# Kernel optimization log

Measured on AMD Instinct MI355X. Metric: run time of the kernel, lower is better.

Reference implementation:

```python
import jax, jax.numpy as jnp
import numpy as np

NEG_SLOPE = 0.2  # PyG GATConv default leaky_relu slope
EPS = 1e-16     # PyG softmax denominator epsilon


def gat_conv(x, src, dst, W, att_src, att_dst, bias, concat, num_nodes):
    """PyG-style GATConv (eval mode, dropout disabled).
    x: [N, F_in]; W: [F_in, H*C]; att_src/att_dst: [H, C]; bias: [H*C] or [C].
    Messages flow src -> dst; softmax is per destination node."""
    H, C = att_src.shape
    h = (x @ W).reshape(num_nodes, H, C)                      # [N,H,C]
    a_src = jnp.sum(h * att_src[None], axis=-1)               # [N,H]
    a_dst = jnp.sum(h * att_dst[None], axis=-1)               # [N,H]
    e = jax.nn.leaky_relu(a_src[src] + a_dst[dst], NEG_SLOPE) # [E,H]
    # numerically-stable segment softmax over edges grouped by dst
    m = jax.ops.segment_max(e, dst, num_segments=num_nodes)   # [N,H]
    ex = jnp.exp(e - m[dst])                                  # [E,H]
    s = jax.ops.segment_sum(ex, dst, num_segments=num_nodes)  # [N,H]
    alpha = ex / (s[dst] + EPS)                               # [E,H]
    msg = h[src] * alpha[..., None]                           # [E,H,C]
    out = jax.ops.segment_sum(msg, dst, num_segments=num_nodes)  # [N,H,C]
    if concat:
        out = out.reshape(num_nodes, H * C)
    else:
        out = out.mean(axis=1)                                # [N,C]
    return out + bias, alpha


def setup_inputs() -> dict:
    key = jax.random.key(0)
    ks = jax.random.split(key, 20)
    N, E = 50000, 500000
    F_node = 128       # num_node_features
    SED = 128          # sentence_embedding_dim
    HID = 64           # hidden_channels
    H = 2              # num_heads

    def g(k, shape, scale=0.05):
        return jax.random.normal(k, shape, dtype=jnp.float32) * scale

    return {
        "x": jax.random.normal(ks[0], (N, SED), dtype=jnp.float32),
        "edge_index": jax.random.randint(ks[1], (2, E), 0, N, dtype=jnp.int64),
        "cls_emb": jax.random.normal(ks[2], (768,), dtype=jnp.float32),
        # fc0: Linear(768, SED)
        "fc0_w": g(ks[3], (SED, 768)), "fc0_b": g(ks[4], (SED,)),
        # conv1: GATConv(2*SED -> HID, heads=H, concat=True)
        "W1": g(ks[5], (2 * SED, H * HID)),
        "att_src1": g(ks[6], (H, HID)), "att_dst1": g(ks[7], (H, HID)),
        "bias1": g(ks[8], (H * HID,)),
        # conv2: GATConv(H*HID -> F_node, heads=H, concat=False)
        "W2": g(ks[9], (H * HID, H * F_node)),
        "att_src2": g(ks[10], (H, F_node)), "att_dst2": g(ks[11], (H, F_node)),
        "bias2": g(ks[12], (F_node,)),
        # edge MLP head
        "fc2_w": g(ks[13], (F_node, 2 * F_node)), "fc2_b": g(ks[14], (F_node,)),
        "fc3_w": g(ks[15], (1, F_node)), "fc3_b": g(ks[16], (1,)),
    }


def reference(x, edge_index, cls_emb, fc0_w, fc0_b,
              W1, att_src1, att_dst1, bias1,
              W2, att_src2, att_dst2, bias2,
              fc2_w, fc2_b, fc3_w, fc3_b):
    N = x.shape[0]
    src, dst = edge_index[0], edge_index[1]
    # sentence embedding projection + broadcast-concat to every node
    sent = fc0_w @ cls_emb + fc0_b                                # [SED]
    h = jnp.concatenate([x, jnp.broadcast_to(sent, (N, sent.shape[0]))], axis=1)
    h, _ = gat_conv(h, src, dst, W1, att_src1, att_dst1, bias1, True, N)
    h = jax.nn.elu(h)
    h, _ = gat_conv(h, src, dst, W2, att_src2, att_dst2, bias2, False, N)
    # edge head: gather endpoints, concat, MLP, sigmoid
    edge_input = jnp.concatenate([h[src], h[dst]], axis=1)        # [E, 2*F]
    z = jax.nn.relu(edge_input @ fc2_w.T + fc2_b)                 # [E, F]
    logits = z @ fc3_w.T + fc3_b                                  # [E, 1]
    return jax.nn.sigmoid(logits)
```

## Files before the change

kernel.cpp:

```cpp
#include <hip/hip_runtime.h>
#include <hip/hip_bf16.h>
#include <math.h>


typedef short short8 __attribute__((ext_vector_type(8)));
typedef float floatx4 __attribute__((ext_vector_type(4)));
typedef float v2f __attribute__((ext_vector_type(2)));
typedef unsigned uint2v __attribute__((ext_vector_type(2)));

__device__ __forceinline__ float wave_allreduce_sum(float v) {
    #pragma unroll
    for (int off = 1; off < 64; off <<= 1) v += __shfl_xor(v, off, 64);
    return v;
}
__device__ __forceinline__ float bf16lo(unsigned u) {
    unsigned x = u << 16; return __builtin_bit_cast(float, x);
}
__device__ __forceinline__ float bf16hi(unsigned u) {
    unsigned x = u & 0xFFFF0000u; return __builtin_bit_cast(float, x);
}
__device__ __forceinline__ v2f bfpair(unsigned v) {
    uint2v t; t.x = v << 16; t.y = v & 0xFFFF0000u;
    return __builtin_bit_cast(v2f, t);
}
__device__ __forceinline__ unsigned short bfbits(float f) {
    return __builtin_bit_cast(unsigned short, __float2bfloat16(f));
}
__device__ __forceinline__ unsigned packbf(float a, float b) {
    return ((unsigned)bfbits(b) << 16) | (unsigned)bfbits(a);
}
__device__ __forceinline__ float lrelu(float v) { return v > 0.f ? v : 0.2f * v; }

__global__ void prep_kernel(const float* __restrict__ cls, const float* __restrict__ fc0_w,
                            const float* __restrict__ fc0_b, const float* __restrict__ W1,
                            const float* __restrict__ W2, const float* __restrict__ fc2_w,
                            float* __restrict__ c1,
                            __hip_bfloat16* __restrict__ w1frag,
                            __hip_bfloat16* __restrict__ w2frag,
                            __hip_bfloat16* __restrict__ fc2frag) {
    int tid = threadIdx.x;
    if (blockIdx.x == 0) {
        __shared__ float s_sent[128];
        if (tid < 128) {
            float acc = fc0_b[tid];
            const float* row = fc0_w + (size_t)tid * 768;
            for (int k = 0; k < 768; ++k) acc += row[k] * cls[k];
            s_sent[tid] = acc;
        }
        __syncthreads();
        if (tid < 128) {
            float acc = 0.f;
            for (int k = 0; k < 128; ++k) acc += s_sent[k] * W1[(128 + k) * 128 + tid];
            c1[tid] = acc;
        }
    }
    int gstride = gridDim.x * blockDim.x;
    int g = blockIdx.x * blockDim.x + tid;
    for (int i = g; i < 16384; i += gstride) {
        int j = i & 7, l = (i >> 3) & 63, nt = (i >> 9) & 7, kt = (i >> 12) & 3;
        int k = kt * 32 + (l >> 4) * 8 + j;
        int n = nt * 16 + (l & 15);
        w1frag[i] = __float2bfloat16(W1[k * 128 + n]);
    }
    for (int i = g; i < 32768; i += gstride) {
        int j = i & 7, l = (i >> 3) & 63, nt = (i >> 9) & 15, kt = (i >> 13) & 3;
        int k = kt * 32 + (l >> 4) * 8 + j;
        int n = nt * 16 + (l & 15);
        w2frag[i] = __float2bfloat16(W2[k * 256 + n]);
    }
    for (int i = g; i < 32768; i += gstride) {
        int j = i & 7, l = (i >> 3) & 63, nt = (i >> 9) & 15, kt = (i >> 13) & 3;
        int k = kt * 32 + (l >> 4) * 8 + j;
        int n = nt * 16 + (l & 15);
        float v = (n < 128) ? fc2_w[n * 256 + k] : fc2_w[(n - 128) * 256 + 128 + k];
        fc2frag[i] = __float2bfloat16(v);
    }
}

__global__ void count_kernel(const int* __restrict__ dst, int* __restrict__ counts, int E) {
    int e = blockIdx.x * blockDim.x + threadIdx.x;
    if (e < E) atomicAdd(&counts[dst[e]], 1);
}

__global__ void __launch_bounds__(1024) scan_kernel(const int* __restrict__ counts,
                                                    int* __restrict__ row, int* __restrict__ woff,
                                                    int N, int E) {
    int tid = threadIdx.x, lane = tid & 63, wv = tid >> 6;
    __shared__ int wsum[16];
    __shared__ int carry;
    if (tid == 0) carry = 0;
    __syncthreads();
    for (int base = 0; base < N; base += 1024) {
        int v = (base + tid < N) ? counts[base + tid] : 0;
        int x = v;
        #pragma unroll
        for (int off = 1; off < 64; off <<= 1) {
            int t = __shfl_up(x, off, 64);
            if (lane >= off) x += t;
        }
        if (lane == 63) wsum[wv] = x;
        __syncthreads();
        if (wv == 0 && lane < 16) {
            int y = wsum[lane];
            #pragma unroll
            for (int off = 1; off < 16; off <<= 1) {
                int t = __shfl_up(y, off, 64);
                if (lane >= off) y += t;
            }
            wsum[lane] = y;
        }
        __syncthreads();
        int wexcl = (wv == 0) ? 0 : wsum[wv - 1];
        int excl = carry + wexcl + x - v;
        if (base + tid < N) { row[base + tid] = excl; woff[base + tid] = excl; }
        __syncthreads();
        if (tid == 0) carry += wsum[15];
        __syncthreads();
    }
    if (tid == 0) row[N] = E;
}

__global__ void scatter_kernel(const int* __restrict__ src, const int* __restrict__ dst,
                               int* __restrict__ woff, int* __restrict__ srcs, int E) {
    int e = blockIdx.x * blockDim.x + threadIdx.x;
    if (e < E) {
        int pos = atomicAdd(&woff[dst[e]], 1);
        srcs[pos] = src[e];
    }
}

__global__ void __launch_bounds__(256) gemm1_mfma_kernel(
        const float* __restrict__ x, const __hip_bfloat16* __restrict__ wfrag,
        const float* __restrict__ c1, const float* __restrict__ att_s, const float* __restrict__ att_d,
        __hip_bfloat16* __restrict__ h1bf, float* __restrict__ a_src, float* __restrict__ a_dst, int N) {
    int lane = threadIdx.x & 63, wv = threadIdx.x >> 6;
    int lo = lane & 15, quad = lane >> 4;
    int rowbase = (blockIdx.x * 4 + wv) * 16;
    if (rowbase >= N) return;
    int arow = rowbase + lo; if (arow >= N) arow = N - 1;
    const float* ap = x + (size_t)arow * 128 + quad * 8;
    floatx4 acc[8];
    #pragma unroll
    for (int nt = 0; nt < 8; ++nt) acc[nt] = (floatx4){0.f, 0.f, 0.f, 0.f};
    const short8* bf = (const short8*)wfrag;
    #pragma unroll
    for (int kt = 0; kt < 4; ++kt) {
        float4 fa = *(const float4*)(ap + kt * 32);
        float4 fb = *(const float4*)(ap + kt * 32 + 4);
        short8 a;
        a[0] = (short)bfbits(fa.x); a[1] = (short)bfbits(fa.y);
        a[2] = (short)bfbits(fa.z); a[3] = (short)bfbits(fa.w);
        a[4] = (short)bfbits(fb.x); a[5] = (short)bfbits(fb.y);
        a[6] = (short)bfbits(fb.z); a[7] = (short)bfbits(fb.w);
        #pragma unroll
        for (int nt = 0; nt < 8; ++nt)
            acc[nt] = __builtin_amdgcn_mfma_f32_16x16x32_bf16(a, bf[(kt * 8 + nt) * 64 + lane], acc[nt], 0, 0, 0);
    }
    float ps0[4] = {0,0,0,0}, ps1[4] = {0,0,0,0}, pd0[4] = {0,0,0,0}, pd1[4] = {0,0,0,0};
    #pragma unroll
    for (int nt = 0; nt < 8; ++nt) {
        int ch = nt * 16 + lo;
        float cv = c1[ch], as_v = att_s[ch], ad_v = att_d[ch];
        #pragma unroll
        for (int r = 0; r < 4; ++r) {
            int row = rowbase + quad * 4 + r;
            float val = acc[nt][r] + cv;
            if (row < N) ((unsigned short*)h1bf)[(size_t)row * 128 + ch] = bfbits(val);
            if (nt < 4) { ps0[r] += val * as_v; pd0[r] += val * ad_v; }
            else        { ps1[r] += val * as_v; pd1[r] += val * ad_v; }
        }
    }
    #pragma unroll
    for (int r = 0; r < 4; ++r) {
        int row = rowbase + quad * 4 + r;
        float v0 = ps0[r], v1 = ps1[r], v2 = pd0[r], v3 = pd1[r];
        #pragma unroll
        for (int off = 1; off < 16; off <<= 1) {
            v0 += __shfl_xor(v0, off, 64); v1 += __shfl_xor(v1, off, 64);
            v2 += __shfl_xor(v2, off, 64); v3 += __shfl_xor(v3, off, 64);
        }
        if (lo == 0 && row < N) {
            a_src[row * 2 + 0] = v0; a_src[row * 2 + 1] = v1;
            a_dst[row * 2 + 0] = v2; a_dst[row * 2 + 1] = v3;
        }
    }
}

__global__ void __launch_bounds__(256) agg1_csr_kernel(
        const int* __restrict__ row, const int* __restrict__ srcs,
        const float* __restrict__ a_src, const float* __restrict__ a_dst,
        const unsigned* __restrict__ h1u, const float* __restrict__ bias1,
        unsigned* __restrict__ hmid_u, int N) {
    int d = blockIdx.x * 4 + (threadIdx.x >> 6);
    if (d >= N) return;
    int lane = threadIdx.x & 63;
    int beg = row[d], end = row[d + 1];
    int g = lane >> 4, q = lane & 15;
    float2 adp = ((const float2*)a_dst)[d];
    float den0 = 0.f, den1 = 0.f;
    v2f facc2[4];
    #pragma unroll
    for (int m = 0; m < 4; ++m) facc2[m] = (v2f){0.f, 0.f};
    for (int b = beg; b < end; b += 64) {
        int i = b + lane;
        int s = 0; float e0 = 0.f, e1 = 0.f;
        if (i < end) {
            s = srcs[i];
            float2 as = ((const float2*)a_src)[s];
            e0 = __expf(lrelu(as.x + adp.x));
            e1 = __expf(lrelu(as.y + adp.y));
            den0 += e0; den1 += e1;
        }
        int cnt = min(64, end - b);
        int rounds = (cnt + 3) >> 2;
        float w0 = __shfl(e0, g, 64);
        float w1 = __shfl(e1, g, 64);
        int   sj = __shfl(s,  g, 64);
        float wgt = (q < 8) ? w0 : w1;
        uint4 u = ((const uint4*)(h1u + (size_t)sj * 64))[q];
        for (int j = 0; j < rounds; ++j) {
            int sl2 = 4 * j + 4 + g; sl2 = sl2 > 63 ? 63 : sl2;
            float w0n = __shfl(e0, sl2, 64);
            float w1n = __shfl(e1, sl2, 64);
            int   sjn = __shfl(s,  sl2, 64);
            uint4 un = ((const uint4*)(h1u + (size_t)sjn * 64))[q];
            float wgtn = (q < 8) ? w0n : w1n;
            facc2[0] += bfpair(u.x) * wgt;
            facc2[1] += bfpair(u.y) * wgt;
            facc2[2] += bfpair(u.z) * wgt;
            facc2[3] += bfpair(u.w) * wgt;
            u = un; wgt = wgtn;
        }
    }
    den0 = wave_allreduce_sum(den0);
    den1 = wave_allreduce_sum(den1);
    #pragma unroll
    for (int m = 0; m < 4; ++m) {
        facc2[m].x += __shfl_xor(facc2[m].x, 16, 64);
        facc2[m].y += __shfl_xor(facc2[m].y, 16, 64);
        facc2[m].x += __shfl_xor(facc2[m].x, 32, 64);
        facc2[m].y += __shfl_xor(facc2[m].y, 32, 64);
    }
    if (lane < 16) {
        float inv = (lane < 8) ? 1.f / (den0 + 1e-16f) : 1.f / (den1 + 1e-16f);
        int c0 = 8 * lane;
        float v[8];
        #pragma unroll
        for (int m = 0; m < 4; ++m) {
            float va = facc2[m].x * inv + bias1[c0 + 2 * m];
            float vb = facc2[m].y * inv + bias1[c0 + 2 * m + 1];
            v[2 * m]     = va > 0.f ? va : expm1f(va);
            v[2 * m + 1] = vb > 0.f ? vb : expm1f(vb);
        }
        uint4 o;
        o.x = packbf(v[0], v[1]); o.y = packbf(v[2], v[3]);
        o.z = packbf(v[4], v[5]); o.w = packbf(v[6], v[7]);
        ((uint4*)(hmid_u + (size_t)d * 64))[lane] = o;
    }
}

__global__ void __launch_bounds__(256) gemm2_mfma_kernel(
        const __hip_bfloat16* __restrict__ hmid, const __hip_bfloat16* __restrict__ wfrag,
        const float* __restrict__ att_s, const float* __restrict__ att_d,
        __hip_bfloat16* __restrict__ h2pre, float* __restrict__ a_src, float* __restrict__ a_dst, int N) {
    int lane = threadIdx.x & 63, wv = threadIdx.x >> 6;
    int lo = lane & 15, quad = lane >> 4;
    int rowbase = (blockIdx.x * 4 + wv) * 16;
    if (rowbase >= N) return;
    int arow = rowbase + lo; if (arow >= N) arow = N - 1;
    const __hip_bfloat16* ap = hmid + (size_t)arow * 128 + quad * 8;
    floatx4 acc[16];
    #pragma unroll
    for (int nt = 0; nt < 16; ++nt) acc[nt] = (floatx4){0.f, 0.f, 0.f, 0.f};
    const short8* bf = (const short8*)wfrag;
    #pragma unroll
    for (int kt = 0; kt < 4; ++kt) {
        short8 a = *(const short8*)(ap + kt * 32);
        #pragma unroll
        for (int nt = 0; nt < 16; ++nt)
            acc[nt] = __builtin_amdgcn_mfma_f32_16x16x32_bf16(a, bf[(kt * 16 + nt) * 64 + lane], acc[nt], 0, 0, 0);
    }
    float ps0[4] = {0,0,0,0}, ps1[4] = {0,0,0,0}, pd0[4] = {0,0,0,0}, pd1[4] = {0,0,0,0};
    #pragma unroll
    for (int nt = 0; nt < 16; ++nt) {
        int ch = nt * 16 + lo;
        float as_v = att_s[ch], ad_v = att_d[ch];
        #pragma unroll
        for (int r = 0; r < 4; ++r) {
            int row = rowbase + quad * 4 + r;
            float val = acc[nt][r];
            if (row < N) ((unsigned short*)h2pre)[(size_t)row * 256 + ch] = bfbits(val);
            if (nt < 8) { ps0[r] += val * as_v; pd0[r] += val * ad_v; }
            else        { ps1[r] += val * as_v; pd1[r] += val * ad_v; }
        }
    }
    #pragma unroll
    for (int r = 0; r < 4; ++r) {
        int row = rowbase + quad * 4 + r;
        float v0 = ps0[r], v1 = ps1[r], v2 = pd0[r], v3 = pd1[r];
        #pragma unroll
        for (int off = 1; off < 16; off <<= 1) {
            v0 += __shfl_xor(v0, off, 64); v1 += __shfl_xor(v1, off, 64);
            v2 += __shfl_xor(v2, off, 64); v3 += __shfl_xor(v3, off, 64);
        }
        if (lo == 0 && row < N) {
            a_src[row * 2 + 0] = v0; a_src[row * 2 + 1] = v1;
            a_dst[row * 2 + 0] = v2; a_dst[row * 2 + 1] = v3;
        }
    }
}

__global__ void __launch_bounds__(256) agg2_csr_kernel(
        const int* __restrict__ row, const int* __restrict__ srcs,
        const float* __restrict__ a_src, const float* __restrict__ a_dst,
        const unsigned* __restrict__ h2u, const float* __restrict__ bias2,
        unsigned* __restrict__ h2bf_u, int N) {
    int d = blockIdx.x * 4 + (threadIdx.x >> 6);
    if (d >= N) return;
    int lane = threadIdx.x & 63;
    int beg = row[d], end = row[d + 1];
    int g = lane >> 5, q = lane & 31;
    float2 adp = ((const float2*)a_dst)[d];
    float den0 = 0.f, den1 = 0.f;
    v2f facc2[4];
    #pragma unroll
    for (int m = 0; m < 4; ++m) facc2[m] = (v2f){0.f, 0.f};
    for (int b = beg; b < end; b += 64) {
        int i = b + lane;
        int s = 0; float e0 = 0.f, e1 = 0.f;
        if (i < end) {
            s = srcs[i];
            float2 as = ((const float2*)a_src)[s];
            e0 = __expf(lrelu(as.x + adp.x));
            e1 = __expf(lrelu(as.y + adp.y));
            den0 += e0; den1 += e1;
        }
        int cnt = min(64, end - b);
        int rounds = (cnt + 1) >> 1;
        float w0 = __shfl(e0, g, 64);
        float w1 = __shfl(e1, g, 64);
        int   sj = __shfl(s,  g, 64);
        float wgt = (q < 16) ? w0 : w1;
        uint4 u = ((const uint4*)(h2u + (size_t)sj * 128))[q];
        for (int j = 0; j < rounds; ++j) {
            int sl2 = 2 * j + 2 + g; sl2 = sl2 > 63 ? 63 : sl2;
            float w0n = __shfl(e0, sl2, 64);
            float w1n = __shfl(e1, sl2, 64);
            int   sjn = __shfl(s,  sl2, 64);
            uint4 un = ((const uint4*)(h2u + (size_t)sjn * 128))[q];
            float wgtn = (q < 16) ? w0n : w1n;
            facc2[0] += bfpair(u.x) * wgt;
            facc2[1] += bfpair(u.y) * wgt;
            facc2[2] += bfpair(u.z) * wgt;
            facc2[3] += bfpair(u.w) * wgt;
            u = un; wgt = wgtn;
        }
    }
    den0 = wave_allreduce_sum(den0);
    den1 = wave_allreduce_sum(den1);
    float inv = (q < 16) ? 0.5f / (den0 + 1e-16f) : 0.5f / (den1 + 1e-16f);
    #pragma unroll
    for (int m = 0; m < 4; ++m) {
        facc2[m].x += __shfl_xor(facc2[m].x, 32, 64);
        facc2[m].y += __shfl_xor(facc2[m].y, 32, 64);
        facc2[m] *= inv;
        facc2[m].x += __shfl_xor(facc2[m].x, 16, 64);
        facc2[m].y += __shfl_xor(facc2[m].y, 16, 64);
    }
    if (lane < 16) {
        int c0 = 8 * lane;
        uint4 o;
        o.x = packbf(facc2[0].x + bias2[c0 + 0], facc2[0].y + bias2[c0 + 1]);
        o.y = packbf(facc2[1].x + bias2[c0 + 2], facc2[1].y + bias2[c0 + 3]);
        o.z = packbf(facc2[2].x + bias2[c0 + 4], facc2[2].y + bias2[c0 + 5]);
        o.w = packbf(facc2[3].x + bias2[c0 + 6], facc2[3].y + bias2[c0 + 7]);
        ((uint4*)(h2bf_u + (size_t)d * 64))[lane] = o;
    }
}

__global__ void __launch_bounds__(256) zsd_mfma_kernel(
        const __hip_bfloat16* __restrict__ h2bf, const __hip_bfloat16* __restrict__ wfrag,
        const float* __restrict__ fc2_b, __hip_bfloat16* __restrict__ zsd, int N) {
    int lane = threadIdx.x & 63, wv = threadIdx.x >> 6;
    int lo = lane & 15, quad = lane >> 4;
    int rowbase = (blockIdx.x * 4 + wv) * 16;
    if (rowbase >= N) return;
    int arow = rowbase + lo; if (arow >= N) arow = N - 1;
    const __hip_bfloat16* ap = h2bf + (size_t)arow * 128 + quad * 8;
    floatx4 acc[16];
    #pragma unroll
    for (int nt = 0; nt < 16; ++nt) acc[nt] = (floatx4){0.f, 0.f, 0.f, 0.f};
    const short8* bf = (const short8*)wfrag;
    #pragma unroll
    for (int kt = 0; kt < 4; ++kt) {
        short8 a = *(const short8*)(ap + kt * 32);
        #pragma unroll
        for (int nt = 0; nt < 16; ++nt)
            acc[nt] = __builtin_amdgcn_mfma_f32_16x16x32_bf16(a, bf[(kt * 16 + nt) * 64 + lane], acc[nt], 0, 0, 0);
    }
    #pragma unroll
    for (int nt = 0; nt < 16; ++nt) {
        int ch = nt * 16 + lo;
        float bv = (nt >= 8) ? fc2_b[ch - 128] : 0.f;
        #pragma unroll
        for (int r = 0; r < 4; ++r) {
            int row = rowbase + quad * 4 + r;
            if (row < N) ((unsigned short*)zsd)[(size_t)row * 256 + ch] = bfbits(acc[nt][r] + bv);
        }
    }
}

__global__ void __launch_bounds__(256) edge_zsd_kernel(
        const int* __restrict__ src, const int* __restrict__ dst,
        const unsigned* __restrict__ zsd_u, const float* __restrict__ fc3_w,
        const float* __restrict__ fc3_b, float* __restrict__ out, int E) {
    int lane = threadIdx.x & 63, wv = threadIdx.x >> 6;
    int g = lane >> 5, r = (lane >> 4) & 1, q = lane & 15;
    int base = (blockIdx.x * 4 + wv) * 16;
    if (base >= E) return;
    v2f f30 = {fc3_w[8 * q + 4 * r + 0], fc3_w[8 * q + 4 * r + 1]};
    v2f f31 = {fc3_w[8 * q + 4 * r + 2], fc3_w[8 * q + 4 * r + 3]};
    float b3 = fc3_b[0];
    #pragma unroll
    for (int j = 0; j < 8; ++j) {
        int e = base + 2 * j + g;
        int ec = e < E ? e : E - 1;
        int node = r ? dst[ec] : src[ec];
        uint4 mine = ((const uint4*)(zsd_u + (size_t)node * 128 + (r << 6)))[q];
        unsigned sx = (unsigned)__shfl_xor((int)mine.x, 16, 64);
        unsigned sy = (unsigned)__shfl_xor((int)mine.y, 16, 64);
        unsigned sz = (unsigned)__shfl_xor((int)mine.z, 16, 64);
        unsigned sw = (unsigned)__shfl_xor((int)mine.w, 16, 64);
        unsigned mA = r ? mine.z : mine.x;
        unsigned mB = r ? mine.w : mine.y;
        unsigned oA = r ? sz : sx;
        unsigned oB = r ? sw : sy;
        v2f sA = bfpair(mA) + bfpair(oA);
        v2f sB = bfpair(mB) + bfpair(oB);
        sA.x = fmaxf(sA.x, 0.f); sA.y = fmaxf(sA.y, 0.f);
        sB.x = fmaxf(sB.x, 0.f); sB.y = fmaxf(sB.y, 0.f);
        v2f p2 = sA * f30 + sB * f31;
        float p = p2.x + p2.y;
        #pragma unroll
        for (int off = 1; off < 32; off <<= 1) p += __shfl_xor(p, off, 64);
        if ((lane & 31) == 0 && e < E)
            out[e] = 1.f / (1.f + expf(-(p + b3)));
    }
}

extern "C" void kernel_launch(void* const* d_in, const int* in_sizes, int n_in,
                              void* d_out, int out_size, void* d_ws, size_t ws_size,
                              hipStream_t stream) {
    const float* x      = (const float*)d_in[0];
    const int*   ei     = (const int*)d_in[1];
    const float* cls    = (const float*)d_in[2];
    const float* fc0_w  = (const float*)d_in[3];
    const float* fc0_b  = (const float*)d_in[4];
    const float* W1     = (const float*)d_in[5];
    const float* att_s1 = (const float*)d_in[6];
    const float* att_d1 = (const float*)d_in[7];
    const float* bias1  = (const float*)d_in[8];
    const float* W2     = (const float*)d_in[9];
    const float* att_s2 = (const float*)d_in[10];
    const float* att_d2 = (const float*)d_in[11];
    const float* bias2  = (const float*)d_in[12];
    const float* fc2_w  = (const float*)d_in[13];
    const float* fc2_b  = (const float*)d_in[14];
    const float* fc3_w  = (const float*)d_in[15];
    const float* fc3_b  = (const float*)d_in[16];
    float* out = (float*)d_out;

    int N = in_sizes[0] / 128;
    int E = in_sizes[1] / 2;
    const int* src = ei;
    const int* dst = ei + E;

    float* w = (float*)d_ws;
    size_t off = 0;
    auto alloc = [&](size_t n) { float* p = w + off; off += (n + 63) & ~(size_t)63; return p; };
    float* c1      = alloc(128);
    float* w1fragf = alloc(16384 / 2);
    float* w2fragf = alloc(32768 / 2);
    float* fc2fragf= alloc(32768 / 2);
    float* a_s1    = alloc((size_t)N * 2);
    float* a_d1    = alloc((size_t)N * 2);
    float* a_s2    = alloc((size_t)N * 2);
    float* a_d2    = alloc((size_t)N * 2);
    float* h1bff   = alloc((size_t)N * 64);
    float* hmidf   = alloc((size_t)N * 64);
    float* h2pref  = alloc((size_t)N * 128);
    float* h2bff   = alloc((size_t)N * 64);
    float* zsdf    = alloc((size_t)N * 128);
    int* counts = (int*)alloc(N);
    int* rowp   = (int*)alloc(N + 1);
    int* woff   = (int*)alloc(N);
    int* srcs   = (int*)alloc(E);
    __hip_bfloat16* w1frag = (__hip_bfloat16*)w1fragf;
    __hip_bfloat16* w2frag = (__hip_bfloat16*)w2fragf;
    __hip_bfloat16* fc2frag= (__hip_bfloat16*)fc2fragf;
    __hip_bfloat16* hmid   = (__hip_bfloat16*)hmidf;
    __hip_bfloat16* h2pre  = (__hip_bfloat16*)h2pref;
    __hip_bfloat16* h2bf   = (__hip_bfloat16*)h2bff;
    __hip_bfloat16* h1bf   = (__hip_bfloat16*)h1bff;
    __hip_bfloat16* zsd    = (__hip_bfloat16*)zsdf;

    hipMemsetAsync(counts, 0, sizeof(int) * (size_t)N, stream);

    prep_kernel<<<64, 256, 0, stream>>>(cls, fc0_w, fc0_b, W1, W2, fc2_w, c1, w1frag, w2frag, fc2frag);
    count_kernel<<<(E + 255) / 256, 256, 0, stream>>>(dst, counts, E);
    scan_kernel<<<1, 1024, 0, stream>>>(counts, rowp, woff, N, E);
    scatter_kernel<<<(E + 255) / 256, 256, 0, stream>>>(src, dst, woff, srcs, E);
    gemm1_mfma_kernel<<<(N + 63) / 64, 256, 0, stream>>>(x, w1frag, c1, att_s1, att_d1, h1bf, a_s1, a_d1, N);
    agg1_csr_kernel<<<(N + 3) / 4, 256, 0, stream>>>(rowp, srcs, a_s1, a_d1, (const unsigned*)h1bf, bias1, (unsigned*)hmid, N);
    gemm2_mfma_kernel<<<(N + 63) / 64, 256, 0, stream>>>(hmid, w2frag, att_s2, att_d2, h2pre, a_s2, a_d2, N);
    agg2_csr_kernel<<<(N + 3) / 4, 256, 0, stream>>>(rowp, srcs, a_s2, a_d2, (const unsigned*)h2pre, bias2, (unsigned*)h2bf, N);
    zsd_mfma_kernel<<<(N + 63) / 64, 256, 0, stream>>>(h2bf, fc2frag, fc2_b, zsd, N);
    edge_zsd_kernel<<<(E + 63) / 64, 256, 0, stream>>>(src, dst, (const unsigned*)zsd, fc3_w, fc3_b, out, E);
}
```

Before: 406.5 us.

## Replace single-block serial CSR scan with three-pass multi-block scan

Replaces the single-block exclusive scan over per-node degree counts with three passes: per-block sums, a one-wave scan of the block sums, and a parallel local scan that adds each block's offset. The aim is to remove the serial chunk loop in one workgroup, which leaves most of the GPU idle. The cost is two extra kernel launches. The top-level scan handles at most 64 blocks, which limits N to 65536 nodes.

```diff
diff --git a/kernel.cpp b/kernel.cpp
--- a/kernel.cpp
+++ b/kernel.cpp
@@ -12,12 +12,6 @@
     #pragma unroll
     for (int off = 1; off < 64; off <<= 1) v += __shfl_xor(v, off, 64);
     return v;
-}
-__device__ __forceinline__ float bf16lo(unsigned u) {
-    unsigned x = u << 16; return __builtin_bit_cast(float, x);
-}
-__device__ __forceinline__ float bf16hi(unsigned u) {
-    unsigned x = u & 0xFFFF0000u; return __builtin_bit_cast(float, x);
 }
 __device__ __forceinline__ v2f bfpair(unsigned v) {
     uint2v t; t.x = v << 16; t.y = v & 0xFFFF0000u;
@@ -82,42 +76,65 @@
     if (e < E) atomicAdd(&counts[dst[e]], 1);
 }
 
-__global__ void __launch_bounds__(1024) scan_kernel(const int* __restrict__ counts,
-                                                    int* __restrict__ row, int* __restrict__ woff,
-                                                    int N, int E) {
+__global__ void __launch_bounds__(256) bsum_kernel(const int* __restrict__ counts,
+                                                   int* __restrict__ bsum, int N) {
+    int base = blockIdx.x * 1024;
+    int tid = threadIdx.x;
+    int v = 0;
+    #pragma unroll
+    for (int k = 0; k < 4; ++k) {
+        int idx = base + k * 256 + tid;
+        if (idx < N) v += counts[idx];
+    }
+    #pragma unroll
+    for (int off = 1; off < 64; off <<= 1) v += __shfl_xor(v, off, 64);
+    __shared__ int ws[4];
+    if ((tid & 63) == 0) ws[tid >> 6] = v;
+    __syncthreads();
+    if (tid == 0) bsum[blockIdx.x] = ws[0] + ws[1] + ws[2] + ws[3];
+}
+
+__global__ void top_scan_kernel(const int* __restrict__ bsum, int* __restrict__ boff, int nb) {
+    int lane = threadIdx.x;
+    int v = (lane < nb) ? bsum[lane] : 0;
+    int x = v;
+    #pragma unroll
+    for (int off = 1; off < 64; off <<= 1) {
+        int t = __shfl_up(x, off, 64);
+        if (lane >= off) x += t;
+    }
+    if (lane < nb) boff[lane] = x - v;
+}
+
+__global__ void __launch_bounds__(1024) local_scan_kernel(const int* __restrict__ counts,
+                                                          const int* __restrict__ boff,
+                                                          int* __restrict__ row, int* __restrict__ woff,
+                                                          int N, int E) {
     int tid = threadIdx.x, lane = tid & 63, wv = tid >> 6;
+    int base = blockIdx.x * 1024;
     __shared__ int wsum[16];
-    __shared__ int carry;
-    if (tid == 0) carry = 0;
+    int v = (base + tid < N) ? counts[base + tid] : 0;
+    int x = v;
+    #pragma unroll
+    for (int off = 1; off < 64; off <<= 1) {
+        int t = __shfl_up(x, off, 64);
+        if (lane >= off) x += t;
+    }
+    if (lane == 63) wsum[wv] = x;
     __syncthreads();
-    for (int base = 0; base < N; base += 1024) {
-        int v = (base + tid < N) ? counts[base + tid] : 0;
-        int x = v;
-        #pragma unroll
-        for (int off = 1; off < 64; off <<= 1) {
-            int t = __shfl_up(x, off, 64);
-            if (lane >= off) x += t;
-        }
-        if (lane == 63) wsum[wv] = x;
-        __syncthreads();
-        if (wv == 0 && lane < 16) {
-            int y = wsum[lane];
-            #pragma unroll
-            for (int off = 1; off < 16; off <<= 1) {
-                int t = __shfl_up(y, off, 64);
-                if (lane >= off) y += t;
-            }
-            wsum[lane] = y;
-        }
-        __syncthreads();
-        int wexcl = (wv == 0) ? 0 : wsum[wv - 1];
-        int excl = carry + wexcl + x - v;
-        if (base + tid < N) { row[base + tid] = excl; woff[base + tid] = excl; }
-        __syncthreads();
-        if (tid == 0) carry += wsum[15];
-        __syncthreads();
-    }
-    if (tid == 0) row[N] = E;
+    if (wv == 0 && lane < 16) {
+        int y = wsum[lane];
+        #pragma unroll
+        for (int off = 1; off < 16; off <<= 1) {
+            int t = __shfl_up(y, off, 64);
+            if (lane >= off) y += t;
+        }
+        wsum[lane] = y;
+    }
+    __syncthreads();
+    int excl = boff[blockIdx.x] + (wv ? wsum[wv - 1] : 0) + x - v;
+    if (base + tid < N) { row[base + tid] = excl; woff[base + tid] = excl; }
+    if (blockIdx.x == 0 && tid == 0) row[N] = E;
 }
 
 __global__ void scatter_kernel(const int* __restrict__ src, const int* __restrict__ dst,
@@ -474,6 +491,7 @@
     int E = in_sizes[1] / 2;
     const int* src = ei;
     const int* dst = ei + E;
+    int nb = (N + 1023) / 1024;
 
     float* w = (float*)d_ws;
     size_t off = 0;
@@ -495,6 +513,8 @@
     int* rowp   = (int*)alloc(N + 1);
     int* woff   = (int*)alloc(N);
     int* srcs   = (int*)alloc(E);
+    int* bsum   = (int*)alloc(64);
+    int* boff   = (int*)alloc(64);
     __hip_bfloat16* w1frag = (__hip_bfloat16*)w1fragf;
     __hip_bfloat16* w2frag = (__hip_bfloat16*)w2fragf;
     __hip_bfloat16* fc2frag= (__hip_bfloat16*)fc2fragf;
@@ -508,7 +528,9 @@
 
     prep_kernel<<<64, 256, 0, stream>>>(cls, fc0_w, fc0_b, W1, W2, fc2_w, c1, w1frag, w2frag, fc2frag);
     count_kernel<<<(E + 255) / 256, 256, 0, stream>>>(dst, counts, E);
-    scan_kernel<<<1, 1024, 0, stream>>>(counts, rowp, woff, N, E);
+    bsum_kernel<<<nb, 256, 0, stream>>>(counts, bsum, N);
+    top_scan_kernel<<<1, 64, 0, stream>>>(bsum, boff, nb);
+    local_scan_kernel<<<nb, 1024, 0, stream>>>(counts, boff, rowp, woff, N, E);
     scatter_kernel<<<(E + 255) / 256, 256, 0, stream>>>(src, dst, woff, srcs, E);
     gemm1_mfma_kernel<<<(N + 63) / 64, 256, 0, stream>>>(x, w1frag, c1, att_s1, att_d1, h1bf, a_s1, a_d1, N);
     agg1_csr_kernel<<<(N + 3) / 4, 256, 0, stream>>>(rowp, srcs, a_s1, a_d1, (const unsigned*)h1bf, bias1, (unsigned*)hmid, N);
```

Result: faster. 361.0 us (-11.2%).
